# Optimization experiments

Hardware: AMD Instinct MI355X
Metric: run time of the kernel (lower is better)

Reference implementation:

```python
import jax, jax.numpy as jnp
import numpy as np

NHEAD, DK, DV = 8, 32, 32
GRAPH = [[1,2,3,6,7],[1,2,4],[1,3,5],[2,4],[3,5],[1,6,8,12],[1,7,9,13],[6,8,10],[7,9,13],[8,10],[9,11],[9,12,14],[11,13,15],[12,14,16],[13,15,17],[14,16],[15,17]]
_idx = np.zeros((17,5), np.int32); _val = np.zeros((17,5), bool)
for _i, _nb in enumerate(GRAPH):
    for _j, _n in enumerate(_nb):
        _idx[_i,_j] = _n-1; _val[_i,_j] = True
NBR_IDX = jnp.asarray(_idx)            # (17,5) neighbor table (pad idx 0)
NBR_VALID = jnp.asarray(_val)          # (17,5) valid-neighbor mask
ATT_MASK = jnp.asarray(np.concatenate([_val, np.ones((17,2), bool)], 1))  # (17,7): 5 local + 2 global keys
INV_SQRT_DK = float(1.0/np.sqrt(DK))

def _ln_c(x, g, b, eps=1e-6):
    # LayerNorm over channel axis of (B,C,L)
    m = x.mean(1, keepdims=True)
    v = x.var(1, keepdims=True)
    return (x - m) * jax.lax.rsqrt(v + eps) * g[None,:,None] + b[None,:,None]

def _bn3(x, g, b, eps=1e-5):
    # BatchNorm1d (training batch stats) per channel over (B,L); x:(B,C,L)
    m = x.mean((0,2), keepdims=True)
    v = x.var((0,2), keepdims=True)
    return (x - m) * jax.lax.rsqrt(v + eps) * g[None,:,None] + b[None,:,None]

def _pos_ffn(x, w1, b1, w2, b2, g, b):
    # x:(B,C,L); Linear over C, relu, Linear back, residual, BatchNorm1d
    h = jax.nn.relu(jnp.einsum('bcl,hc->bhl', x, w1) + b1[None,:,None])
    y = jnp.einsum('bhl,ch->bcl', h, w2) + b2[None,:,None] + x
    return _bn3(y, g, b)

def _unfold(t):
    # t:(B,C,17) -> (B,C,5,17): per-node 5-wide neighbor window, zero padded
    g = t[:,:,NBR_IDX]                              # (B,C,17,5)
    g = jnp.where(NBR_VALID[None,None], g, 0.0)
    return jnp.transpose(g, (0,1,3,2))

def _sju(xn, ax, wq,bq,wk,bk,wv,bv, bng,bnb, f1w,f1b,f2w,f2b,fg,fb):
    B, C, L = xn.shape
    q = (jnp.einsum('oc,bcl->bol', wq, xn) + bq[None,:,None]).reshape(B,NHEAD,DK,L)
    kx = jnp.einsum('oc,bcl->bol', wk, xn) + bk[None,:,None]
    vx = jnp.einsum('oc,bcl->bol', wv, xn) + bv[None,:,None]
    k = _unfold(kx).reshape(B,NHEAD,DK,5,L)
    v = _unfold(vx).reshape(B,NHEAD,DV,5,L)
    ak = (jnp.einsum('oc,bcal->boal', wk, ax) + bk[None,:,None,None]).reshape(B,NHEAD,DK,2,L)
    av = (jnp.einsum('oc,bcal->boal', wv, ax) + bv[None,:,None,None]).reshape(B,NHEAD,DV,2,L)
    k = jnp.concatenate([k, ak], 3)                 # (B,H,dk,7,L)
    v = jnp.concatenate([v, av], 3)
    pre = jnp.einsum('bhdl,bhdwl->bhwl', q, k) * INV_SQRT_DK
    pre = jnp.where(ATT_MASK.T[None,None], pre, -jnp.inf)
    a = jax.nn.softmax(pre, axis=2)
    att = jnp.einsum('bhwl,bhdwl->bhdl', a, v).reshape(B,C,L)
    ret = _bn3(xn + att, bng, bnb)
    return _pos_ffn(ret, f1w,f1b,f2w,f2b,fg,fb)

def _sru(x, y, wq,bq,wk,bk,wv,bv, bng,bnb, f1w,f1b,f2w,f2b,fg,fb):
    # x:(B,C) relay, y:(B,C,Ly) keys/values
    B, C = x.shape
    q = (x @ wq.T + bq).reshape(B,NHEAD,DK)
    k = (jnp.einsum('oc,bcl->bol', wk, y) + bk[None,:,None]).reshape(B,NHEAD,DK,-1)
    v = (jnp.einsum('oc,bcl->bol', wv, y) + bv[None,:,None]).reshape(B,NHEAD,DV,-1)
    a = jax.nn.softmax(jnp.einsum('bhd,bhdl->bhl', q, k) * INV_SQRT_DK, axis=2)
    att = jnp.einsum('bhl,bhdl->bhd', a, v).reshape(B,C)
    ret = _bn3((x + att)[:,:,None], bng, bnb)
    return _pos_ffn(ret, f1w,f1b,f2w,f2b,fg,fb)[:,:,0]

def _forward(data, ln_g, ln_b, jq_w, jq_b, jk_w, jk_b, jv_w, jv_b, jbn_g, jbn_b, jf1_w, jf1_b, jf2_w, jf2_b, jfbn_g, jfbn_b, rq_w, rq_b, rk_w, rk_b, rv_w, rv_b, rbn_g, rbn_b, rf1_w, rf1_b, rf2_w, rf2_b, rfbn_g, rfbn_b):
    B, C, V, T = data.shape
    embs = jnp.transpose(data, (0,3,1,2)).reshape(B*T, C, V)   # fold time into batch
    nodes = embs
    relay = embs.mean(2)                                       # (BT,C)
    # ax: per node the 2 extra keys = its own original embedding + relay (fixed across layers)
    ax = jnp.stack([embs, jnp.broadcast_to(relay[:,:,None], embs.shape)], axis=2)  # (BT,C,2,V)
    for i in range(ln_g.shape[0]):
        xn = _ln_c(nodes, ln_g[i], ln_b[i])
        nodes = jax.nn.leaky_relu(_sju(xn, ax, jq_w[i],jq_b[i],jk_w[i],jk_b[i],jv_w[i],jv_b[i],jbn_g[i],jbn_b[i],jf1_w[i],jf1_b[i],jf2_w[i],jf2_b[i],jfbn_g[i],jfbn_b[i]), 0.01)
        y = jnp.concatenate([relay[:,:,None], nodes], axis=2)   # (BT,C,18)
        relay = jax.nn.leaky_relu(_sru(relay, y, rq_w[i],rq_b[i],rk_w[i],rk_b[i],rv_w[i],rv_b[i],rbn_g[i],rbn_b[i],rf1_w[i],rf1_b[i],rf2_w[i],rf2_b[i],rfbn_g[i],rfbn_b[i]), 0.01)
    return jnp.transpose(nodes.reshape(B,T,C,V), (0,2,3,1))

def setup_inputs():
    key = jax.random.key(0)
    Lyr, C, DIN, B, T, V = 2, 256, 1024, 4, 256, 17
    ks = jax.random.split(key, 40)
    ctr = [0]
    def nxt():
        k = ks[ctr[0]]; ctr[0] += 1; return k
    def w(shape, s=0.05):
        return jax.random.normal(nxt(), shape, jnp.float32) * s
    ones = lambda: jnp.ones((Lyr, C), jnp.float32)
    zeros = lambda: jnp.zeros((Lyr, C), jnp.float32)
    inp = {'data': jax.random.normal(nxt(), (B,C,V,T), jnp.float32),
           'ln_g': ones(), 'ln_b': zeros()}
    for p in ('j', 'r'):
        inp[p+'q_w'] = w((Lyr,C,C)); inp[p+'q_b'] = w((Lyr,C))
        inp[p+'k_w'] = w((Lyr,C,C)); inp[p+'k_b'] = w((Lyr,C))
        inp[p+'v_w'] = w((Lyr,C,C)); inp[p+'v_b'] = w((Lyr,C))
        inp[p+'bn_g'] = ones(); inp[p+'bn_b'] = zeros()
        inp[p+'f1_w'] = w((Lyr,DIN,C)); inp[p+'f1_b'] = w((Lyr,DIN))
        inp[p+'f2_w'] = w((Lyr,C,DIN)); inp[p+'f2_b'] = w((Lyr,C))
        inp[p+'fbn_g'] = ones(); inp[p+'fbn_b'] = zeros()
    return inp

def reference(data, ln_g, ln_b, jq_w, jq_b, jk_w, jk_b, jv_w, jv_b, jbn_g, jbn_b, jf1_w, jf1_b, jf2_w, jf2_b, jfbn_g, jfbn_b, rq_w, rq_b, rk_w, rk_b, rv_w, rv_b, rbn_g, rbn_b, rf1_w, rf1_b, rf2_w, rf2_b, rfbn_g, rfbn_b):
    return _forward(data, ln_g, ln_b, jq_w, jq_b, jk_w, jk_b, jv_w, jv_b, jbn_g, jbn_b, jf1_w, jf1_b, jf2_w, jf2_b, jfbn_g, jfbn_b, rq_w, rq_b, rk_w, rk_b, rv_w, rv_b, rbn_g, rbn_b, rf1_w, rf1_b, rf2_w, rf2_b, rfbn_g, rfbn_b)
```

## Files before the change

### kernel.cpp

```cpp
#include <hip/hip_runtime.h>
#include <hip/hip_bf16.h>


using bf16 = __hip_bfloat16;
typedef __attribute__((ext_vector_type(8))) short bf16x8v;
typedef __attribute__((ext_vector_type(4))) float f32x4;

namespace {
constexpr int kBT = 1024;
constexpr int kC = 256;
constexpr int kV = 17;
constexpr int kT = 256;
constexpr int kDIN = 1024;
constexpr int kRows = kBT * kV;
constexpr int kRowsE = kRows + kBT;
constexpr float kInvSqrtDk = 0.17677669529663687f;
constexpr size_t SZ_BIG = (size_t)kRows * kC;
}

__constant__ int c_nbi[17][5] = {
    {0, 1, 2, 5, 6},   {0, 1, 3, 0, 0},   {0, 2, 4, 0, 0},  {1, 3, 0, 0, 0},
    {2, 4, 0, 0, 0},   {0, 5, 7, 11, 0},  {0, 6, 8, 12, 0}, {5, 7, 9, 0, 0},
    {6, 8, 12, 0, 0},  {7, 9, 0, 0, 0},   {8, 10, 0, 0, 0}, {8, 11, 13, 0, 0},
    {10, 12, 14, 0, 0},{11, 13, 15, 0, 0},{12, 14, 16, 0, 0},
    {13, 15, 0, 0, 0}, {14, 16, 0, 0, 0}};
__constant__ int c_ncnt[17] = {5, 3, 3, 2, 2, 4, 4, 3, 3, 2, 2, 3, 3, 3, 3, 2, 2};

__device__ inline float bf2f(unsigned short s) {
  unsigned int u = ((unsigned int)s) << 16;
  float f;
  __builtin_memcpy(&f, &u, 4);
  return f;
}
__device__ inline unsigned short f2bf(float f) {
  unsigned int u;
  __builtin_memcpy(&u, &f, 4);
  unsigned int r = (u + 0x7fffu + ((u >> 16) & 1u)) >> 16;
  return (unsigned short)r;
}
__device__ inline float4 ldbf4(const bf16* p) {
  ushort4 u = *(const ushort4*)p;
  return make_float4(bf2f(u.x), bf2f(u.y), bf2f(u.z), bf2f(u.w));
}
__device__ inline void stbf4(bf16* p, float4 v) {
  ushort4 u = make_ushort4(f2bf(v.x), f2bf(v.y), f2bf(v.z), f2bf(v.w));
  *(ushort4*)p = u;
}
__device__ inline float dot4(float4 a, float4 b) {
  return a.x * b.x + a.y * b.y + a.z * b.z + a.w * b.w;
}

__device__ inline void async16(const bf16* g, bf16* l) {
  __builtin_amdgcn_global_load_lds(
      (const __attribute__((address_space(1))) void*)g,
      (__attribute__((address_space(3))) void*)l, 16, 0, 0);
}

template <int KT>
__device__ __forceinline__ void gemm128_body(
    char* smem_raw, const bf16* __restrict__ A, const bf16* __restrict__ W,
    const float* __restrict__ bias, bf16* __restrict__ outB, int N, int flags,
    int row0, int col0) {
  bf16* As = (bf16*)smem_raw;
  bf16* Bs = (bf16*)(smem_raw + 16384);
  const int tid = threadIdx.x;
  const int wave = tid >> 6;
  const int lane = tid & 63;

  const int sub = lane >> 2;
  const int kq = (lane & 3) * 8;
  const int rg0 = (2 * wave + 0) * 16;
  const int rg1 = (2 * wave + 1) * 16;
  const bf16* ag0 = A + (size_t)(row0 + rg0 + sub) * KT + kq;
  const bf16* ag1 = A + (size_t)(row0 + rg1 + sub) * KT + kq;
  const bf16* bg0 = W + (size_t)(col0 + rg0 + sub) * KT + kq;
  const bf16* bg1 = W + (size_t)(col0 + rg1 + sub) * KT + kq;

  const int wm = wave >> 1, wn = wave & 1;
  const int fr = lane & 15;
  const int fk = (lane >> 4) * 8;

  f32x4 acc[4][4];
#pragma unroll
  for (int i = 0; i < 4; ++i)
#pragma unroll
    for (int j = 0; j < 4; ++j) acc[i][j] = (f32x4){0.f, 0.f, 0.f, 0.f};

#define STAGE32(buf, koff)                              \
  do {                                                  \
    async16(ag0 + (koff), As + (buf) * 4096 + rg0 * 32); \
    async16(ag1 + (koff), As + (buf) * 4096 + rg1 * 32); \
    async16(bg0 + (koff), Bs + (buf) * 4096 + rg0 * 32); \
    async16(bg1 + (koff), Bs + (buf) * 4096 + rg1 * 32); \
  } while (0)

  STAGE32(0, 0);
  __syncthreads();

  for (int k0 = 0; k0 < KT; k0 += 32) {
    const int cur = (k0 >> 5) & 1;
    if (k0 + 32 < KT) STAGE32(cur ^ 1, k0 + 32);
    bf16x8v af[4], bfv[4];
#pragma unroll
    for (int i = 0; i < 4; ++i)
      af[i] = *(const bf16x8v*)&As[cur * 4096 +
                                   (wm * 64 + i * 16 + fr) * 32 + fk];
#pragma unroll
    for (int j = 0; j < 4; ++j)
      bfv[j] = *(const bf16x8v*)&Bs[cur * 4096 +
                                    (wn * 64 + j * 16 + fr) * 32 + fk];
#pragma unroll
    for (int i = 0; i < 4; ++i)
#pragma unroll
      for (int j = 0; j < 4; ++j)
        acc[i][j] = __builtin_amdgcn_mfma_f32_16x16x32_bf16(af[i], bfv[j],
                                                            acc[i][j], 0, 0,
                                                            0);
    __syncthreads();
  }
#undef STAGE32

  unsigned short* cs = (unsigned short*)smem_raw;
#pragma unroll
  for (int j = 0; j < 4; ++j) {
    int lc = wn * 64 + j * 16 + fr;
    float bv = bias ? bias[col0 + lc] : 0.f;
#pragma unroll
    for (int i = 0; i < 4; ++i) {
      int lr = wm * 64 + i * 16 + (lane >> 4) * 4;
#pragma unroll
      for (int r = 0; r < 4; ++r) {
        float v = acc[i][j][r] + bv;
        if (flags & 1) v = fmaxf(v, 0.f);
        cs[(lr + r) * 128 + lc] = f2bf(v);
      }
    }
  }
  __syncthreads();
#pragma unroll
  for (int p = 0; p < 8; ++p) {
    int lr = p * 16 + (tid >> 4);
    int lc = (tid & 15) * 8;
    *(bf16x8v*)&outB[(size_t)(row0 + lr) * N + col0 + lc] =
        *(const bf16x8v*)&cs[lr * 128 + lc];
  }
}

template <int KT>
__global__ __launch_bounds__(256, 4) void k_mfma_gemm(
    const bf16* __restrict__ A, const bf16* __restrict__ W,
    const float* __restrict__ bias, bf16* __restrict__ outB, int N,
    int flags) {
  __shared__ __align__(16) char smem_raw[32768];
  gemm128_body<KT>(smem_raw, A, W, bias, outB, N, flags, blockIdx.x * 128,
                   blockIdx.y * 128);
}

__global__ __launch_bounds__(256, 4) void k_mfma_gemm_dual(
    const bf16* __restrict__ A0, const bf16* __restrict__ W0,
    const float* __restrict__ b0, bf16* __restrict__ o0, int N0, int gx0,
    int nb0, const bf16* __restrict__ A1, const bf16* __restrict__ W1,
    const float* __restrict__ b1, bf16* __restrict__ o1, int N1, int gx1) {
  __shared__ __align__(16) char smem_raw[32768];
  const int bid = blockIdx.x;
  if (bid < nb0) {
    int bx = bid % gx0, by = bid / gx0;
    gemm128_body<256>(smem_raw, A0, W0, b0, o0, N0, 4, bx * 128, by * 128);
  } else {
    int local = bid - nb0;
    int bx = local % gx1, by = local / gx1;
    gemm128_body<256>(smem_raw, A1, W1, b1, o1, N1, 4, bx * 128, by * 128);
  }
}

__global__ __launch_bounds__(256, 4) void k_mfma_gemm64(
    const bf16* __restrict__ A, const bf16* __restrict__ W,
    const float* __restrict__ bias, const float* __restrict__ res,
    float* __restrict__ outF, const float* __restrict__ bnScI,
    const float* __restrict__ bnShI, float* __restrict__ partOut, int nbPart,
    int N) {
  constexpr int KT = 1024;
  __shared__ __align__(16) bf16 As[2][4096];
  __shared__ __align__(16) bf16 Bs[2][4096];
  __shared__ float sred[4 * 64];
  __shared__ float qred[4 * 64];
  const int tid = threadIdx.x;
  const int wave = tid >> 6;
  const int lane = tid & 63;
  const int row0 = blockIdx.x * 64;
  const int col0 = blockIdx.y * 64;

  const int srow = wave * 16 + (lane >> 2);
  const int skq = (lane & 3) * 8;
  const bf16* ag = A + (size_t)(row0 + srow) * KT + skq;
  const bf16* bg = W + (size_t)(col0 + srow) * KT + skq;

  const int wm = wave >> 1, wn = wave & 1;
  const int fr = lane & 15;
  const int fk = (lane >> 4) * 8;

  f32x4 acc[2][2];
#pragma unroll
  for (int i = 0; i < 2; ++i)
#pragma unroll
    for (int j = 0; j < 2; ++j) acc[i][j] = (f32x4){0.f, 0.f, 0.f, 0.f};

#define STAGE64x64(buf, koff)                                      \
  do {                                                             \
    _Pragma("unroll") for (int kc = 0; kc < 2; ++kc) {             \
      async16(ag + (koff) + kc * 32,                               \
              &As[(buf)][kc * 2048 + wave * 512]);                 \
      async16(bg + (koff) + kc * 32,                               \
              &Bs[(buf)][kc * 2048 + wave * 512]);                 \
    }                                                              \
  } while (0)

  STAGE64x64(0, 0);
  __syncthreads();

  for (int k0 = 0; k0 < KT; k0 += 64) {
    const int cur = (k0 >> 6) & 1;
    if (k0 + 64 < KT) STAGE64x64(cur ^ 1, k0 + 64);
#pragma unroll
    for (int kc = 0; kc < 2; ++kc) {
      bf16x8v af[2], bfv[2];
#pragma unroll
      for (int i = 0; i < 2; ++i)
        af[i] = *(const bf16x8v*)&As[cur][kc * 2048 +
                                          (wm * 32 + i * 16 + fr) * 32 + fk];
#pragma unroll
      for (int j = 0; j < 2; ++j)
        bfv[j] = *(const bf16x8v*)&Bs[cur][kc * 2048 +
                                           (wn * 32 + j * 16 + fr) * 32 + fk];
#pragma unroll
      for (int i = 0; i < 2; ++i)
#pragma unroll
        for (int j = 0; j < 2; ++j)
          acc[i][j] = __builtin_amdgcn_mfma_f32_16x16x32_bf16(af[i], bfv[j],
                                                              acc[i][j], 0, 0,
                                                              0);
    }
    __syncthreads();
  }
#undef STAGE64x64

  const int crow = row0 + wm * 32;
  const int ccol = col0 + wn * 32;
  float colS[2] = {0.f, 0.f};
  float colQ[2] = {0.f, 0.f};
#pragma unroll
  for (int j = 0; j < 2; ++j) {
    int col = ccol + j * 16 + fr;
    float bv = bias[col];
    float rsc = bnScI[col], rsh = bnShI[col];
#pragma unroll
    for (int i = 0; i < 2; ++i) {
      int rowb = crow + i * 16 + (lane >> 4) * 4;
#pragma unroll
      for (int r = 0; r < 4; ++r) {
        size_t row = (size_t)(rowb + r);
        float v = acc[i][j][r] + bv + res[row * N + col] * rsc + rsh;
        outF[row * N + col] = v;
        colS[j] += v;
        colQ[j] += v * v;
      }
    }
  }
#pragma unroll
  for (int j = 0; j < 2; ++j) {
    colS[j] += __shfl_xor(colS[j], 16);
    colS[j] += __shfl_xor(colS[j], 32);
    colQ[j] += __shfl_xor(colQ[j], 16);
    colQ[j] += __shfl_xor(colQ[j], 32);
  }
  if (lane < 16) {
#pragma unroll
    for (int j = 0; j < 2; ++j) {
      sred[wave * 64 + j * 16 + fr] = colS[j];
      qred[wave * 64 + j * 16 + fr] = colQ[j];
    }
  }
  __syncthreads();
  if (tid < 64) {
    int c = tid;
    int wsel = c >> 5, off = c & 31;
    float s = sred[wsel * 64 + off] + sred[(wsel + 2) * 64 + off];
    float q = qred[wsel * 64 + off] + qred[(wsel + 2) * 64 + off];
    int col = col0 + c;
    partOut[(size_t)blockIdx.x * kC + col] = s;
    partOut[(size_t)(nbPart + blockIdx.x) * kC + col] = q;
  }
}

__global__ __launch_bounds__(256) void k_xform_in(const float* __restrict__ data,
                                                  float* __restrict__ nodes,
                                                  bf16* __restrict__ embs_bf) {
  __shared__ float tile[32][33];
  int ct = blockIdx.x * 32, tt = blockIdx.y * 32;
  int bv = blockIdx.z;
  int b = bv / kV, v = bv - b * kV;
  int tx = threadIdx.x & 31, ty = threadIdx.x >> 5;
  for (int i = ty; i < 32; i += 8)
    tile[i][tx] = data[(((size_t)b * kC + ct + i) * kV + v) * kT + tt + tx];
  __syncthreads();
  for (int i = ty; i < 32; i += 8) {
    size_t s = (size_t)b * kT + tt + i;
    size_t idx = (s * kV + v) * kC + ct + tx;
    float val = tile[tx][i];
    nodes[idx] = val;
    embs_bf[idx] = __float2bfloat16(val);
  }
}

__global__ __launch_bounds__(256) void k_xform_out(const float* __restrict__ Z,
                                                   const float* __restrict__ scale,
                                                   const float* __restrict__ shift,
                                                   float* __restrict__ out) {
  __shared__ float tile[32][33];
  int ct = blockIdx.x * 32, tt = blockIdx.y * 32;
  int bv = blockIdx.z;
  int b = bv / kV, v = bv - b * kV;
  int tx = threadIdx.x & 31, ty = threadIdx.x >> 5;
  float sc = scale[ct + tx], sh = shift[ct + tx];
  for (int i = ty; i < 32; i += 8) {
    size_t s = (size_t)b * kT + tt + i;
    float val = Z[(s * kV + v) * kC + ct + tx] * sc + sh;
    val = (val > 0.f) ? val : 0.01f * val;
    tile[i][tx] = val;
  }
  __syncthreads();
  for (int i = ty; i < 32; i += 8)
    out[(((size_t)b * kC + ct + i) * kV + v) * kT + tt + tx] = tile[tx][i];
}

__global__ __launch_bounds__(256) void k_ln_relay(
    const float* __restrict__ nodes, const float* __restrict__ g,
    const float* __restrict__ b, float* __restrict__ O,
    bf16* __restrict__ Ob, bf16* __restrict__ relay0_bf) {
  int t = threadIdx.x;
  int bid = blockIdx.x;
  if (bid < kRows / 4) {
    int row = bid * 4 + (t >> 6);
    int c4 = (t & 63) * 4;
    size_t i = (size_t)row * kC + c4;
    float4 x = *(const float4*)(nodes + i);
    float s = x.x + x.y + x.z + x.w;
    float q = dot4(x, x);
#pragma unroll
    for (int o = 32; o >= 1; o >>= 1) {
      s += __shfl_xor(s, o);
      q += __shfl_xor(q, o);
    }
    float m = s * (1.f / 256.f);
    float var = q * (1.f / 256.f) - m * m;
    float rs = rsqrtf(var + 1e-6f);
    float4 g4 = *(const float4*)(g + c4);
    float4 b4 = *(const float4*)(b + c4);
    float4 o4 = make_float4((x.x - m) * rs * g4.x + b4.x,
                            (x.y - m) * rs * g4.y + b4.y,
                            (x.z - m) * rs * g4.z + b4.z,
                            (x.w - m) * rs * g4.w + b4.w);
    *(float4*)(O + i) = o4;
    stbf4(Ob + i, o4);
  } else {
    int s = (bid - kRows / 4) * 4 + (t >> 6);
    int c4 = (t & 63) * 4;
    float4 acc = make_float4(0.f, 0.f, 0.f, 0.f);
#pragma unroll
    for (int v = 0; v < kV; ++v) {
      float4 x = *(const float4*)(nodes + ((size_t)s * kV + v) * kC + c4);
      acc.x += x.x; acc.y += x.y; acc.z += x.z; acc.w += x.w;
    }
    float4 r =
        make_float4(acc.x / 17.f, acc.y / 17.f, acc.z / 17.f, acc.w / 17.f);
    stbf4(relay0_bf + (size_t)s * kC + c4, r);
  }
}

__global__ __launch_bounds__(256) void k_attn_sat(const bf16* __restrict__ qkv,
                                                  const bf16* __restrict__ akav,
                                                  float* __restrict__ z,
                                                  float* __restrict__ part,
                                                  int nb) {
  __shared__ float sS[4][256];
  __shared__ float qS[4][256];
  int t = threadIdx.x;
  int w = t >> 6;
  int rl = blockIdx.x * 4 + w;
  int lane = t & 63;
  int s = rl / kV, l = rl - s * kV;
  int c4 = lane * 4;
  float4 q = ldbf4(qkv + (size_t)rl * 768 + c4);
  int cnt = c_ncnt[l];
  float sc[7];
  int nrow[5];
#pragma unroll
  for (int wd = 0; wd < 5; ++wd) {
    nrow[wd] = s * kV + c_nbi[l][wd];
    float4 k = ldbf4(qkv + (size_t)nrow[wd] * 768 + 256 + c4);
    float p = dot4(q, k);
    p += __shfl_xor(p, 1, 8);
    p += __shfl_xor(p, 2, 8);
    p += __shfl_xor(p, 4, 8);
    sc[wd] = (wd < cnt) ? p * kInvSqrtDk : -1e30f;
  }
  {
    float4 k = ldbf4(akav + (size_t)rl * 1024 + c4);
    float p = dot4(q, k);
    p += __shfl_xor(p, 1, 8);
    p += __shfl_xor(p, 2, 8);
    p += __shfl_xor(p, 4, 8);
    sc[5] = p * kInvSqrtDk;
  }
  {
    float4 k = ldbf4(akav + (size_t)(kRows + s) * 1024 + c4);
    float p = dot4(q, k);
    p += __shfl_xor(p, 1, 8);
    p += __shfl_xor(p, 2, 8);
    p += __shfl_xor(p, 4, 8);
    sc[6] = p * kInvSqrtDk;
  }
  float mx = sc[0];
#pragma unroll
  for (int wd = 1; wd < 7; ++wd) mx = fmaxf(mx, sc[wd]);
  float den = 0.f;
#pragma unroll
  for (int wd = 0; wd < 7; ++wd) {
    sc[wd] = __expf(sc[wd] - mx);
    den += sc[wd];
  }
  float inv = 1.f / den;
  float4 acc = make_float4(0.f, 0.f, 0.f, 0.f);
#pragma unroll
  for (int wd = 0; wd < 5; ++wd) {
    float4 v = ldbf4(qkv + (size_t)nrow[wd] * 768 + 512 + c4);
    acc.x += sc[wd] * v.x; acc.y += sc[wd] * v.y;
    acc.z += sc[wd] * v.z; acc.w += sc[wd] * v.w;
  }
  {
    float4 v = ldbf4(akav + (size_t)rl * 1024 + 256 + c4);
    acc.x += sc[5] * v.x; acc.y += sc[5] * v.y;
    acc.z += sc[5] * v.z; acc.w += sc[5] * v.w;
  }
  {
    float4 v = ldbf4(akav + (size_t)(kRows + s) * 1024 + 256 + c4);
    acc.x += sc[6] * v.x; acc.y += sc[6] * v.y;
    acc.z += sc[6] * v.z; acc.w += sc[6] * v.w;
  }
  size_t zi = (size_t)rl * kC + c4;
  float4 xv = *(const float4*)(z + zi);
  float4 o = make_float4(xv.x + acc.x * inv, xv.y + acc.y * inv,
                         xv.z + acc.z * inv, xv.w + acc.w * inv);
  *(float4*)(z + zi) = o;
  sS[w][c4 + 0] = o.x; sS[w][c4 + 1] = o.y;
  sS[w][c4 + 2] = o.z; sS[w][c4 + 3] = o.w;
  qS[w][c4 + 0] = o.x * o.x; qS[w][c4 + 1] = o.y * o.y;
  qS[w][c4 + 2] = o.z * o.z; qS[w][c4 + 3] = o.w * o.w;
  __syncthreads();
  float ps = sS[0][t] + sS[1][t] + sS[2][t] + sS[3][t];
  float pq = qS[0][t] + qS[1][t] + qS[2][t] + qS[3][t];
  part[(size_t)blockIdx.x * kC + t] = ps;
  part[(size_t)(nb + blockIdx.x) * kC + t] = pq;
}

__global__ __launch_bounds__(256) void k_bn_finalize(const float* __restrict__ part,
                                                     int nb, float inv_n,
                                                     const float* __restrict__ g,
                                                     const float* __restrict__ b,
                                                     float* __restrict__ scale,
                                                     float* __restrict__ shift) {
  int c = blockIdx.x;
  int t = threadIdx.x;
  float s = 0.f, q = 0.f;
  for (int i = t; i < nb; i += 256) {
    s += part[(size_t)i * kC + c];
    q += part[(size_t)(nb + i) * kC + c];
  }
#pragma unroll
  for (int o = 32; o >= 1; o >>= 1) {
    s += __shfl_xor(s, o);
    q += __shfl_xor(q, o);
  }
  __shared__ float ws[4], wq[4];
  int wid = t >> 6;
  if ((t & 63) == 0) { ws[wid] = s; wq[wid] = q; }
  __syncthreads();
  if (t == 0) {
    float S = ws[0] + ws[1] + ws[2] + ws[3];
    float Q = wq[0] + wq[1] + wq[2] + wq[3];
    float m = S * inv_n;
    float var = Q * inv_n - m * m;
    float sc = g[c] * rsqrtf(var + 1e-5f);
    scale[c] = sc;
    shift[c] = b[c] - m * sc;
  }
}

__global__ __launch_bounds__(256) void k_bn_apply(const float* __restrict__ Z,
                                                  const float* __restrict__ scale,
                                                  const float* __restrict__ shift,
                                                  float* __restrict__ outF,
                                                  bf16* __restrict__ outB,
                                                  int leaky) {
  int t = threadIdx.x;
  int row = blockIdx.x * 4 + (t >> 6);
  int c4 = (t & 63) * 4;
  size_t i = (size_t)row * kC + c4;
  float4 z = *(const float4*)(Z + i);
  float4 sc = *(const float4*)(scale + c4);
  float4 sh = *(const float4*)(shift + c4);
  float4 v = make_float4(z.x * sc.x + sh.x, z.y * sc.y + sh.y,
                         z.z * sc.z + sh.z, z.w * sc.w + sh.w);
  if (leaky) {
    v.x = (v.x > 0.f) ? v.x : 0.01f * v.x;
    v.y = (v.y > 0.f) ? v.y : 0.01f * v.y;
    v.z = (v.z > 0.f) ? v.z : 0.01f * v.z;
    v.w = (v.w > 0.f) ? v.w : 0.01f * v.w;
  }
  if (outF) *(float4*)(outF + i) = v;
  if (outB) stbf4(outB + i, v);
}

__global__ __launch_bounds__(256) void k_bn_ln(
    const float* __restrict__ Z, const float* __restrict__ scale,
    const float* __restrict__ shift, const float* __restrict__ g,
    const float* __restrict__ b, float* __restrict__ xnOut,
    bf16* __restrict__ actOut) {
  int t = threadIdx.x;
  int row = blockIdx.x * 4 + (t >> 6);
  int c4 = (t & 63) * 4;
  size_t i = (size_t)row * kC + c4;
  float4 z = *(const float4*)(Z + i);
  float4 sc = *(const float4*)(scale + c4);
  float4 sh = *(const float4*)(shift + c4);
  float4 v = make_float4(z.x * sc.x + sh.x, z.y * sc.y + sh.y,
                         z.z * sc.z + sh.z, z.w * sc.w + sh.w);
  v.x = (v.x > 0.f) ? v.x : 0.01f * v.x;
  v.y = (v.y > 0.f) ? v.y : 0.01f * v.y;
  v.z = (v.z > 0.f) ? v.z : 0.01f * v.z;
  v.w = (v.w > 0.f) ? v.w : 0.01f * v.w;
  float s = v.x + v.y + v.z + v.w;
  float q = dot4(v, v);
#pragma unroll
  for (int o = 32; o >= 1; o >>= 1) {
    s += __shfl_xor(s, o);
    q += __shfl_xor(q, o);
  }
  float m = s * (1.f / 256.f);
  float var = q * (1.f / 256.f) - m * m;
  float rs = rsqrtf(var + 1e-6f);
  float4 g4 = *(const float4*)(g + c4);
  float4 b4 = *(const float4*)(b + c4);
  float4 o4 = make_float4((v.x - m) * rs * g4.x + b4.x,
                          (v.y - m) * rs * g4.y + b4.y,
                          (v.z - m) * rs * g4.z + b4.z,
                          (v.w - m) * rs * g4.w + b4.w);
  *(float4*)(xnOut + i) = o4;
  stbf4(actOut + i, o4);
}

struct CvtTab {
  const float* src[12];
  bf16* dst[12];
  int n[12];
  const float* bsrc[10];
  float* bdst[10];
};
__global__ __launch_bounds__(256) void k_cvt_multi(CvtTab t) {
  int c = blockIdx.y;
  if (c == 12) {
    if (blockIdx.x < 10) t.bdst[blockIdx.x][threadIdx.x] = t.bsrc[blockIdx.x][threadIdx.x];
    return;
  }
  int i = (blockIdx.x * 256 + threadIdx.x) * 4;
  if (i >= t.n[c]) return;
  float4 v = *(const float4*)(t.src[c] + i);
  stbf4(t.dst[c] + i, v);
}

extern "C" void kernel_launch(void* const* d_in, const int* in_sizes, int n_in,
                              void* d_out, int out_size, void* d_ws, size_t ws_size,
                              hipStream_t stream) {
  const float* data = (const float*)d_in[0];
  const float* ln_g = (const float*)d_in[1];
  const float* ln_b = (const float*)d_in[2];
  const float* jq_w = (const float*)d_in[3];
  const float* jq_b = (const float*)d_in[4];
  const float* jk_w = (const float*)d_in[5];
  const float* jk_b = (const float*)d_in[6];
  const float* jv_w = (const float*)d_in[7];
  const float* jv_b = (const float*)d_in[8];
  const float* jbn_g = (const float*)d_in[9];
  const float* jbn_b = (const float*)d_in[10];
  const float* jf1_w = (const float*)d_in[11];
  const float* jf1_b = (const float*)d_in[12];
  const float* jf2_w = (const float*)d_in[13];
  const float* jf2_b = (const float*)d_in[14];
  const float* jfbn_g = (const float*)d_in[15];
  const float* jfbn_b = (const float*)d_in[16];
  float* out = (float*)d_out;

  float* f = (float*)d_ws;
  float* nodes = f;    f += SZ_BIG;
  float* xn = f;       f += SZ_BIG;
  float* part = f;     f += 2 * (kRows / 4) * kC;
  float* scale = f;    f += kC;
  float* shift = f;    f += kC;
  float* cb_jqkv = f;  f += 2 * 768;
  float* cb_kv4 = f;   f += 1024;

  bf16* bfa = (bf16*)f;
  bf16* act_bf = bfa;   bfa += SZ_BIG;
  bf16* embsX_bf = bfa; bfa += (size_t)kRowsE * kC;
  bf16* P = bfa;        bfa += (size_t)kRows * kDIN;
  bf16* akavBuf = bfa;  bfa += (size_t)kRowsE * 1024;
  bf16* Wjqkv = bfa;    bfa += 2 * 768 * 256;
  bf16* Wkv4 = bfa;     bfa += 1024 * 256;
  bf16* Wjf1 = bfa;     bfa += 2 * 1024 * 256;
  bf16* Wjf2 = bfa;     bfa += 2 * 256 * 1024;

  bf16* relay0_bf = embsX_bf + SZ_BIG;
  bf16* qkv_bf = P;
  bf16* h_bf = P;
  float* y2 = xn;

  auto gemm = [&](const bf16* A, const bf16* W, const float* bias,
                  bf16* oB, int M, int N, int flags) {
    dim3 g(M / 128, N / 128);
    k_mfma_gemm<256><<<g, 256, 0, stream>>>(A, W, bias, oB, N, flags);
  };

  {
    CvtTab t;
    for (int i = 0; i < 2; ++i) {
      const size_t om = (size_t)i * kC * kC;
      const float* s3[3] = {jq_w + om, jk_w + om, jv_w + om};
      bf16* d3[3] = {Wjqkv + (size_t)i * 768 * 256,
                     Wjqkv + (size_t)i * 768 * 256 + 65536,
                     Wjqkv + (size_t)i * 768 * 256 + 131072};
      for (int j = 0; j < 3; ++j) {
        t.src[i * 3 + j] = s3[j];
        t.dst[i * 3 + j] = d3[j];
        t.n[i * 3 + j] = 65536;
      }
    }
    t.src[6] = jk_w;                 t.dst[6] = Wkv4;               t.n[6] = 65536;
    t.src[7] = jv_w;                 t.dst[7] = Wkv4 + 65536;       t.n[7] = 65536;
    t.src[8] = jk_w + (size_t)65536; t.dst[8] = Wkv4 + 131072;      t.n[8] = 65536;
    t.src[9] = jv_w + (size_t)65536; t.dst[9] = Wkv4 + 196608;      t.n[9] = 65536;
    t.src[10] = jf1_w; t.dst[10] = Wjf1; t.n[10] = 2 * 1024 * 256;
    t.src[11] = jf2_w; t.dst[11] = Wjf2; t.n[11] = 2 * 256 * 1024;
    for (int i = 0; i < 2; ++i) {
      t.bsrc[i * 3 + 0] = jq_b + (size_t)i * kC;
      t.bsrc[i * 3 + 1] = jk_b + (size_t)i * kC;
      t.bsrc[i * 3 + 2] = jv_b + (size_t)i * kC;
      t.bdst[i * 3 + 0] = cb_jqkv + i * 768;
      t.bdst[i * 3 + 1] = cb_jqkv + i * 768 + 256;
      t.bdst[i * 3 + 2] = cb_jqkv + i * 768 + 512;
    }
    t.bsrc[6] = jk_b;       t.bdst[6] = cb_kv4;
    t.bsrc[7] = jv_b;       t.bdst[7] = cb_kv4 + 256;
    t.bsrc[8] = jk_b + kC;  t.bdst[8] = cb_kv4 + 512;
    t.bsrc[9] = jv_b + kC;  t.bdst[9] = cb_kv4 + 768;
    k_cvt_multi<<<dim3(512, 13), 256, 0, stream>>>(t);
  }

  k_xform_in<<<dim3(8, 8, 4 * kV), 256, 0, stream>>>(data, nodes, embsX_bf);

  k_ln_relay<<<kRows / 4 + kBT / 4, 256, 0, stream>>>(nodes, ln_g, ln_b, xn,
                                                      act_bf, relay0_bf);

  {
    const int gx0 = kRowsE / 128, nb0 = gx0 * (1024 / 128);
    const int gx1 = kRows / 128, nb1 = gx1 * (768 / 128);
    k_mfma_gemm_dual<<<nb0 + nb1, 256, 0, stream>>>(
        embsX_bf, Wkv4, cb_kv4, akavBuf, 1024, gx0, nb0,
        act_bf, Wjqkv, cb_jqkv, qkv_bf, 768, gx1);
  }

  for (int i = 0; i < 2; ++i) {
    const size_t ob = (size_t)i * kC, ofb1 = (size_t)i * kDIN;
    const bf16* Wf1 = Wjf1 + (size_t)i * 1024 * 256;
    const bf16* Wf2 = Wjf2 + (size_t)i * 256 * 1024;
    const int nbA = kRows / 4;
    const int nbG = kRows / 64;

    if (i == 1) {
      gemm(act_bf, Wjqkv + (size_t)768 * 256, cb_jqkv + 768, qkv_bf, kRows,
           768, 4);
    }
    k_attn_sat<<<kRows / 4, 256, 0, stream>>>(qkv_bf, akavBuf + (size_t)i * 512,
                                              xn, part, nbA);
    k_bn_finalize<<<kC, 256, 0, stream>>>(part, nbA, 1.f / kRows, jbn_g + ob,
                                          jbn_b + ob, scale, shift);
    k_bn_apply<<<kRows / 4, 256, 0, stream>>>(xn, scale, shift, nullptr,
                                              act_bf, 0);
    gemm(act_bf, Wf1, jf1_b + ofb1, h_bf, kRows, 1024, 4 | 1);
    k_mfma_gemm64<<<dim3(kRows / 64, kC / 64), 256, 0, stream>>>(
        h_bf, Wf2, jf2_b + ob, xn, y2, scale, shift, part, nbG, kC);
    k_bn_finalize<<<kC, 256, 0, stream>>>(part, nbG, 1.f / kRows, jfbn_g + ob,
                                          jfbn_b + ob, scale, shift);
    if (i == 0) {
      k_bn_ln<<<kRows / 4, 256, 0, stream>>>(y2, scale, shift, ln_g + kC,
                                             ln_b + kC, xn, act_bf);
    }
  }

  k_xform_out<<<dim3(8, 8, 4 * kV), 256, 0, stream>>>(y2, scale, shift, out);
  (void)in_sizes; (void)n_in; (void)out_size; (void)ws_size;
}
```

Before: 398.2 us.

## Stage full K=256 tiles into LDS at once in 128x128 GEMM

The K=256 GEMM kernels now issue all eight 32-wide K chunks of A and W into LDS up front (128 KB of shared memory) and run the MFMA loop with a single barrier. The per-iteration double-buffer barriers are gone. In exchange, each workgroup uses 128 KB of LDS and launch bounds drop to 1 block per CU, which cuts occupancy and removes any overlap between loading and compute inside a block.

Measured after the change: 445.0 us. 1.12x slower.

```diff
diff --git a/kernel.cpp b/kernel.cpp
--- a/kernel.cpp
+++ b/kernel.cpp
@@ -56,13 +56,13 @@
       (__attribute__((address_space(3))) void*)l, 16, 0, 0);
 }
 
-template <int KT>
-__device__ __forceinline__ void gemm128_body(
+__device__ __forceinline__ void gemm128_fullk_body(
     char* smem_raw, const bf16* __restrict__ A, const bf16* __restrict__ W,
     const float* __restrict__ bias, bf16* __restrict__ outB, int N, int flags,
     int row0, int col0) {
+  constexpr int KT = 256;
   bf16* As = (bf16*)smem_raw;
-  bf16* Bs = (bf16*)(smem_raw + 16384);
+  bf16* Bs = (bf16*)(smem_raw + 65536);
   const int tid = threadIdx.x;
   const int wave = tid >> 6;
   const int lane = tid & 63;
@@ -80,34 +80,32 @@
   const int fr = lane & 15;
   const int fk = (lane >> 4) * 8;
 
+#pragma unroll
+  for (int kc = 0; kc < 8; ++kc) {
+    const int off = kc * 32;
+    async16(ag0 + off, As + kc * 4096 + rg0 * 32);
+    async16(ag1 + off, As + kc * 4096 + rg1 * 32);
+    async16(bg0 + off, Bs + kc * 4096 + rg0 * 32);
+    async16(bg1 + off, Bs + kc * 4096 + rg1 * 32);
+  }
+  __syncthreads();
+
   f32x4 acc[4][4];
 #pragma unroll
   for (int i = 0; i < 4; ++i)
 #pragma unroll
     for (int j = 0; j < 4; ++j) acc[i][j] = (f32x4){0.f, 0.f, 0.f, 0.f};
 
-#define STAGE32(buf, koff)                              \
-  do {                                                  \
-    async16(ag0 + (koff), As + (buf) * 4096 + rg0 * 32); \
-    async16(ag1 + (koff), As + (buf) * 4096 + rg1 * 32); \
-    async16(bg0 + (koff), Bs + (buf) * 4096 + rg0 * 32); \
-    async16(bg1 + (koff), Bs + (buf) * 4096 + rg1 * 32); \
-  } while (0)
-
-  STAGE32(0, 0);
-  __syncthreads();
-
-  for (int k0 = 0; k0 < KT; k0 += 32) {
-    const int cur = (k0 >> 5) & 1;
-    if (k0 + 32 < KT) STAGE32(cur ^ 1, k0 + 32);
+#pragma unroll
+  for (int kc = 0; kc < 8; ++kc) {
     bf16x8v af[4], bfv[4];
 #pragma unroll
     for (int i = 0; i < 4; ++i)
-      af[i] = *(const bf16x8v*)&As[cur * 4096 +
+      af[i] = *(const bf16x8v*)&As[kc * 4096 +
                                    (wm * 64 + i * 16 + fr) * 32 + fk];
 #pragma unroll
     for (int j = 0; j < 4; ++j)
-      bfv[j] = *(const bf16x8v*)&Bs[cur * 4096 +
+      bfv[j] = *(const bf16x8v*)&Bs[kc * 4096 +
                                     (wn * 64 + j * 16 + fr) * 32 + fk];
 #pragma unroll
     for (int i = 0; i < 4; ++i)
@@ -116,9 +114,8 @@
         acc[i][j] = __builtin_amdgcn_mfma_f32_16x16x32_bf16(af[i], bfv[j],
                                                             acc[i][j], 0, 0,
                                                             0);
-    __syncthreads();
-  }
-#undef STAGE32
+  }
+  __syncthreads();
 
   unsigned short* cs = (unsigned short*)smem_raw;
 #pragma unroll
@@ -146,30 +143,29 @@
   }
 }
 
-template <int KT>
-__global__ __launch_bounds__(256, 4) void k_mfma_gemm(
+__global__ __launch_bounds__(256, 1) void k_mfma_gemm(
     const bf16* __restrict__ A, const bf16* __restrict__ W,
     const float* __restrict__ bias, bf16* __restrict__ outB, int N,
     int flags) {
-  __shared__ __align__(16) char smem_raw[32768];
-  gemm128_body<KT>(smem_raw, A, W, bias, outB, N, flags, blockIdx.x * 128,
-                   blockIdx.y * 128);
-}
-
-__global__ __launch_bounds__(256, 4) void k_mfma_gemm_dual(
+  __shared__ __align__(16) char smem_raw[131072];
+  gemm128_fullk_body(smem_raw, A, W, bias, outB, N, flags, blockIdx.x * 128,
+                     blockIdx.y * 128);
+}
+
+__global__ __launch_bounds__(256, 1) void k_mfma_gemm_dual(
     const bf16* __restrict__ A0, const bf16* __restrict__ W0,
     const float* __restrict__ b0, bf16* __restrict__ o0, int N0, int gx0,
     int nb0, const bf16* __restrict__ A1, const bf16* __restrict__ W1,
     const float* __restrict__ b1, bf16* __restrict__ o1, int N1, int gx1) {
-  __shared__ __align__(16) char smem_raw[32768];
+  __shared__ __align__(16) char smem_raw[131072];
   const int bid = blockIdx.x;
   if (bid < nb0) {
     int bx = bid % gx0, by = bid / gx0;
-    gemm128_body<256>(smem_raw, A0, W0, b0, o0, N0, 4, bx * 128, by * 128);
+    gemm128_fullk_body(smem_raw, A0, W0, b0, o0, N0, 4, bx * 128, by * 128);
   } else {
     int local = bid - nb0;
     int bx = local % gx1, by = local / gx1;
-    gemm128_body<256>(smem_raw, A1, W1, b1, o1, N1, 4, bx * 128, by * 128);
+    gemm128_fullk_body(smem_raw, A1, W1, b1, o1, N1, 4, bx * 128, by * 128);
   }
 }
 
@@ -627,7 +623,7 @@
   auto gemm = [&](const bf16* A, const bf16* W, const float* bias,
                   bf16* oB, int M, int N, int flags) {
     dim3 g(M / 128, N / 128);
-    k_mfma_gemm<256><<<g, 256, 0, stream>>>(A, W, bias, oB, N, flags);
+    k_mfma_gemm<<<g, 256, 0, stream>>>(A, W, bias, oB, N, flags);
   };
 
   {
```
